# Performance work log

Hardware: AMD Instinct MI355X
Metric: run time of the kernel (lower is better)

## Reference

```python
import jax, jax.numpy as jnp
import numpy as np

T, H, I, E, K = 4096, 2048, 1408, 8, 2  # tokens, hidden, intermediate, experts, top_k


def setup_inputs() -> dict:
    key = jax.random.key(0)
    ks = jax.random.split(key, 6)
    hidden_states = jax.random.normal(ks[0], (T, H), dtype=jnp.float32)
    gate_weight = jax.random.normal(ks[1], (E, H), dtype=jnp.float32) * 0.02  # fp32 gate, per source assert
    w13_weight = jax.random.randint(ks[2], (E, 2 * I, H), -127, 128, dtype=jnp.int8)
    w13_weight_scale = jax.random.uniform(ks[3], (E, 2 * I), dtype=jnp.float32, minval=0.5, maxval=1.5) * 0.005
    w2_weight = jax.random.randint(ks[4], (E, H, I), -127, 128, dtype=jnp.int8)
    w2_weight_scale = jax.random.uniform(ks[5], (E, H), dtype=jnp.float32, minval=0.5, maxval=1.5) * 0.005
    return dict(hidden_states=hidden_states, gate_weight=gate_weight,
                w13_weight=w13_weight, w13_weight_scale=w13_weight_scale,
                w2_weight=w2_weight, w2_weight_scale=w2_weight_scale)


def _dynamic_quant_i8(x):
    # per-token dynamic symmetric int8: scale = max|x|/127 (smooth scales default to ones)
    s = jnp.maximum(jnp.max(jnp.abs(x), axis=-1, keepdims=True) / 127.0, 1e-8)
    q = jnp.clip(jnp.round(x / s), -127.0, 127.0)
    return q, s


def reference(hidden_states, gate_weight, w13_weight, w13_weight_scale, w2_weight, w2_weight_scale):
    # --- gating: fp32 linear + topk softmax (renormalize=True) ---
    logits = hidden_states @ gate_weight.T              # [T, E]
    probs = jax.nn.softmax(logits, axis=-1)
    topv, topi = jax.lax.top_k(probs, K)                # [T, K]
    gates = topv / jnp.sum(topv, axis=-1, keepdims=True)
    # dense routing weights [T, E]: gate value where expert selected, else 0
    route = jnp.zeros((T, E), hidden_states.dtype).at[jnp.arange(T)[:, None], topi].add(gates)

    # --- dynamic per-token int8 quant of routed input (same token value for each of its K copies) ---
    q_in, s_in = _dynamic_quant_i8(hidden_states)       # [T, H], [T, 1]

    # --- grouped w8a8 GEMM (fc1) -> SwiGLU -> requant -> grouped GEMM (fc2) -> weighted combine ---
    def step(acc, xs):
        w13, s13, w2, s2w, r = xs                       # per-expert weights / route column [T]
        h1 = (q_in @ w13.T.astype(jnp.float32)) * s_in * s13[None, :]   # dequant fc1: [T, 2I]
        g, u = h1[:, :I], h1[:, I:]
        act = jax.nn.silu(g) * u                        # SwiGLU
        q_a, s_a = _dynamic_quant_i8(act)
        h2 = (q_a @ w2.T.astype(jnp.float32)) * s_a * s2w[None, :]      # dequant fc2: [T, H]
        return acc + r[:, None] * h2, None

    acc0 = jnp.zeros_like(hidden_states)
    out, _ = jax.lax.scan(step, acc0,
                          (w13_weight, w13_weight_scale, w2_weight, w2_weight_scale, route.T))
    return out
```

## Files before the change

### kernel.cpp

```cpp
#include <hip/hip_runtime.h>

#define T_TOK 4096
#define H_DIM 2048
#define I_DIM 1408
#define E_NUM 8
#define NI2   (2 * I_DIM)

typedef int v4i __attribute__((ext_vector_type(4)));

#define GLD_LDS16(gptr, lptr)                                                        \
  __builtin_amdgcn_global_load_lds(                                                  \
      (const __attribute__((address_space(1))) void*)(gptr),                         \
      (__attribute__((address_space(3))) void*)(lptr), 16, 0, 0)

__global__ __launch_bounds__(256) void pack_all(const int* __restrict__ w13,
                                                const int* __restrict__ w2,
                                                signed char* __restrict__ qw13,
                                                signed char* __restrict__ qw2,
                                                int n16a, int n16tot) {
  int i = blockIdx.x * 256 + threadIdx.x;
  if (i >= n16tot) return;
  const int* src;
  signed char* dst;
  int j;
  if (i < n16a) { src = w13; dst = qw13; j = i; }
  else          { src = w2;  dst = qw2;  j = i - n16a; }
  const int4* s4 = (const int4*)src + (size_t)j * 4;
  int4 v0 = s4[0], v1 = s4[1], v2 = s4[2], v3 = s4[3];
  union { signed char c[16]; int4 v; } pk;
  pk.c[0] = (signed char)v0.x;  pk.c[1] = (signed char)v0.y;
  pk.c[2] = (signed char)v0.z;  pk.c[3] = (signed char)v0.w;
  pk.c[4] = (signed char)v1.x;  pk.c[5] = (signed char)v1.y;
  pk.c[6] = (signed char)v1.z;  pk.c[7] = (signed char)v1.w;
  pk.c[8] = (signed char)v2.x;  pk.c[9] = (signed char)v2.y;
  pk.c[10] = (signed char)v2.z; pk.c[11] = (signed char)v2.w;
  pk.c[12] = (signed char)v3.x; pk.c[13] = (signed char)v3.y;
  pk.c[14] = (signed char)v3.z; pk.c[15] = (signed char)v3.w;
  ((int4*)dst)[j] = pk.v;
}

__global__ __launch_bounds__(256) void gate_route_quant(
    const float* __restrict__ hs, const float* __restrict__ gw,
    signed char* __restrict__ qin, float* __restrict__ s_in,
    int* __restrict__ tope, float* __restrict__ gts) {
  const int t = blockIdx.x;
  const int tid = threadIdx.x;
  const int lane = tid & 63;
  const int wave = tid >> 6;
  const float* row = hs + (size_t)t * H_DIM;

  const float4* r4 = (const float4*)row + tid * 2;
  float4 xa = r4[0], xb = r4[1];
  float x[8] = {xa.x, xa.y, xa.z, xa.w, xb.x, xb.y, xb.z, xb.w};

  double pd[8];
  for (int e = 0; e < 8; e++) pd[e] = 0.0;
  float am = 0.f;
  for (int j = 0; j < 8; j++) {
    float v = x[j];
    am = fmaxf(am, fabsf(v));
    int col = tid * 8 + j;
    for (int e = 0; e < 8; e++)
      pd[e] += (double)v * (double)gw[e * H_DIM + col];
  }
  for (int e = 0; e < 8; e++)
    for (int s = 32; s; s >>= 1) pd[e] += __shfl_down(pd[e], s);
  for (int s = 32; s; s >>= 1) am = fmaxf(am, __shfl_down(am, s));

  __shared__ double sred[4][8];
  __shared__ float sam[4];
  __shared__ float sbc;
  if (lane == 0) {
    for (int e = 0; e < 8; e++) sred[wave][e] = pd[e];
    sam[wave] = am;
  }
  __syncthreads();
  if (tid == 0) {
    float l[8];
    for (int e = 0; e < 8; e++)
      l[e] = (float)(sred[0][e] + sred[1][e] + sred[2][e] + sred[3][e]);
    float amx = fmaxf(fmaxf(sam[0], sam[1]), fmaxf(sam[2], sam[3]));
    float s = fmaxf(amx / 127.0f, 1e-8f);
    s_in[t] = s;
    sbc = s;
    int i1 = 0;
    for (int e = 1; e < 8; e++) if (l[e] > l[i1]) i1 = e;
    int i2 = -1;
    for (int e = 0; e < 8; e++) {
      if (e == i1) continue;
      if (i2 < 0 || l[e] > l[i2]) i2 = e;
    }
    float d = expf(l[i2] - l[i1]);
    tope[2 * t] = i1;     gts[2 * t] = 1.0f / (1.0f + d);
    tope[2 * t + 1] = i2; gts[2 * t + 1] = d / (1.0f + d);
  }
  __syncthreads();
  float s = sbc;
  union { signed char c[8]; unsigned long long u; } pk;
  for (int j = 0; j < 8; j++) {
    float q = rintf(x[j] / s);
    q = fminf(127.f, fmaxf(-127.f, q));
    pk.c[j] = (signed char)q;
  }
  ((unsigned long long*)(qin + (size_t)t * H_DIM))[tid] = pk.u;
}

__global__ __launch_bounds__(256) void build_lists(
    const int* __restrict__ tope, int* __restrict__ tok_list,
    int* __restrict__ epos, int* __restrict__ cnt) {
  __shared__ int lc[E_NUM];
  __shared__ int lbase[E_NUM];
  const int tid = threadIdx.x;
  if (tid < E_NUM) lc[tid] = 0;
  __syncthreads();
  const int t = blockIdx.x * 256 + tid;
  int e0 = tope[2 * t], e1 = tope[2 * t + 1];
  int p0 = atomicAdd(&lc[e0], 1);
  int p1 = atomicAdd(&lc[e1], 1);
  __syncthreads();
  if (tid < E_NUM) lbase[tid] = atomicAdd(&cnt[tid], lc[tid]);
  __syncthreads();
  int pos0 = lbase[e0] + p0;
  int pos1 = lbase[e1] + p1;
  tok_list[e0 * T_TOK + pos0] = t;
  tok_list[e1 * T_TOK + pos1] = t;
  epos[2 * t] = (e0 << 16) | pos0;
  epos[2 * t + 1] = (e1 << 16) | pos1;
}

__global__ void calc_off(const int* __restrict__ cnt, int* __restrict__ off) {
  if (threadIdx.x == 0) {
    int s = 0;
    for (int e = 0; e < E_NUM; e++) { off[e] = s; s += cnt[e]; }
  }
}

__global__ __launch_bounds__(256, 4) void gemm1_silu(
    const signed char* __restrict__ qw13, const signed char* __restrict__ qin,
    const float* __restrict__ s_in, const float* __restrict__ s13,
    const int* __restrict__ tok_list, const int* __restrict__ cnt,
    const int* __restrict__ off, float* __restrict__ act,
    unsigned int* __restrict__ amax) {
  const int bid = blockIdx.x;
  const int e = bid & 7;
  const int xt = bid >> 9;
  const int yt = (bid >> 3) & 63;
  const int ce = cnt[e];
  const int m0 = yt * 64;
  if (m0 >= ce) return;
  const int n0 = xt * 64;

  __shared__ __align__(16) signed char As[64 * 64];
  __shared__ __align__(16) signed char Bg[64 * 64];
  __shared__ __align__(16) signed char Bu[64 * 64];

  const int tid = threadIdx.x;
  const int lane = tid & 63;
  const int wave = tid >> 6;
  const int quad = lane >> 4;
  const int ln = lane & 15;

  const int* tl = tok_list + e * T_TOK;
  const int rowA = tid >> 2;
  const int kc = (tid & 3) * 16;

  const int tA = tl[min(m0 + rowA, ce - 1)];
  const signed char* gA = qin + (size_t)tA * H_DIM + kc;
  const signed char* w13e = qw13 + (size_t)e * NI2 * H_DIM;
  const signed char* gBg = w13e + (size_t)(n0 + rowA) * H_DIM + kc;
  const signed char* gBu = gBg + (size_t)I_DIM * H_DIM;
  const int ldsA = tid * 16;

  v4i accg[4], accu[4];
  v4i zero = {0, 0, 0, 0};
#pragma unroll
  for (int i = 0; i < 4; i++) { accg[i] = zero; accu[i] = zero; }

  for (int k0 = 0; k0 < H_DIM; k0 += 64) {
    __syncthreads();
    GLD_LDS16(gA + k0, As + ldsA);
    GLD_LDS16(gBg + k0, Bg + ldsA);
    GLD_LDS16(gBu + k0, Bu + ldsA);
    __syncthreads();

    v4i af[4], bg, bu;
#pragma unroll
    for (int mt = 0; mt < 4; mt++)
      af[mt] = *(const v4i*)(As + (mt * 16 + ln) * 64 + quad * 16);
    bg = *(const v4i*)(Bg + (wave * 16 + ln) * 64 + quad * 16);
    bu = *(const v4i*)(Bu + (wave * 16 + ln) * 64 + quad * 16);
#pragma unroll
    for (int mt = 0; mt < 4; mt++) {
      accg[mt] = __builtin_amdgcn_mfma_i32_16x16x64_i8(af[mt], bg, accg[mt], 0, 0, 0);
      accu[mt] = __builtin_amdgcn_mfma_i32_16x16x64_i8(af[mt], bu, accu[mt], 0, 0, 0);
    }
  }

  const float* s13e = s13 + e * NI2;
  const int n = n0 + wave * 16 + ln;
  const float sgv = s13e[n];
  const float suv = s13e[I_DIM + n];
  const int offe = off[e];
#pragma unroll
  for (int mt = 0; mt < 4; mt++) {
#pragma unroll
    for (int r = 0; r < 4; r++) {
      int mrel = m0 + mt * 16 + quad * 4 + r;
      bool valid = mrel < ce;
      int tok = tl[valid ? mrel : 0];
      float si = s_in[tok];
      int crow = offe + mrel;
      float g = (float)accg[mt][r] * si * sgv;
      float u = (float)accu[mt][r] * si * suv;
      float a = g / (1.0f + expf(-g)) * u;
      if (valid) act[(size_t)crow * I_DIM + n] = a;
      float am = fabsf(a);
      for (int s = 1; s < 16; s <<= 1) am = fmaxf(am, __shfl_xor(am, s, 16));
      if (valid && ln == 0) atomicMax(amax + crow, __float_as_uint(am));
    }
  }
}

__global__ __launch_bounds__(256) void quant_act(const float* __restrict__ act,
                                                 const unsigned int* __restrict__ amax,
                                                 signed char* __restrict__ qa,
                                                 float* __restrict__ s_a) {
  const int r = blockIdx.x;
  float am = __uint_as_float(amax[r]);
  float s = fmaxf(am / 127.0f, 1e-8f);
  if (threadIdx.x == 0) s_a[r] = s;
  const float* arow = act + (size_t)r * I_DIM;
  signed char* qrow = qa + (size_t)r * I_DIM;
  for (int j = threadIdx.x; j < I_DIM; j += 256) {
    float q = rintf(arow[j] / s);
    q = fminf(127.f, fmaxf(-127.f, q));
    qrow[j] = (signed char)q;
  }
}

__global__ __launch_bounds__(256, 4) void gemm2_h2(
    const signed char* __restrict__ qw2, const signed char* __restrict__ qa,
    const float* __restrict__ s_a, const float* __restrict__ s2w,
    const int* __restrict__ cnt, const int* __restrict__ off,
    float* __restrict__ h2s) {
  const int bid = blockIdx.x;
  const int e = bid & 7;
  const int xt = bid >> 9;
  const int yt = (bid >> 3) & 63;
  const int ce = cnt[e];
  const int m0 = yt * 64;
  if (m0 >= ce) return;
  const int n0 = xt * 128;
  const int offe = off[e];

  __shared__ __align__(16) signed char As[64 * 64];
  __shared__ __align__(16) signed char Bs[128 * 64];

  const int tid = threadIdx.x;
  const int lane = tid & 63;
  const int wave = tid >> 6;
  const int quad = lane >> 4;
  const int ln = lane & 15;

  const int rowA = tid >> 2;
  const int kc = (tid & 3) * 16;

  const signed char* gA = qa + (size_t)(offe + min(m0 + rowA, ce - 1)) * I_DIM + kc;
  const signed char* w2e = qw2 + (size_t)e * H_DIM * I_DIM;
  const signed char* gB0 = w2e + (size_t)(n0 + rowA) * I_DIM + kc;
  const signed char* gB1 = gB0 + (size_t)64 * I_DIM;
  const int ldsA = tid * 16;
  const int lds1 = 4096 + ldsA;

  v4i acc[4][2];
  v4i zero = {0, 0, 0, 0};
#pragma unroll
  for (int i = 0; i < 4; i++)
#pragma unroll
    for (int j = 0; j < 2; j++) acc[i][j] = zero;

  for (int k0 = 0; k0 < I_DIM; k0 += 64) {
    __syncthreads();
    GLD_LDS16(gA + k0, As + ldsA);
    GLD_LDS16(gB0 + k0, Bs + ldsA);
    GLD_LDS16(gB1 + k0, Bs + lds1);
    __syncthreads();

    v4i af[4], bf[2];
#pragma unroll
    for (int mt = 0; mt < 4; mt++)
      af[mt] = *(const v4i*)(As + (mt * 16 + ln) * 64 + quad * 16);
#pragma unroll
    for (int nt = 0; nt < 2; nt++)
      bf[nt] = *(const v4i*)(Bs + (wave * 32 + nt * 16 + ln) * 64 + quad * 16);
#pragma unroll
    for (int mt = 0; mt < 4; mt++)
#pragma unroll
      for (int nt = 0; nt < 2; nt++)
        acc[mt][nt] = __builtin_amdgcn_mfma_i32_16x16x64_i8(af[mt], bf[nt], acc[mt][nt], 0, 0, 0);
  }

  const float* s2e = s2w + e * H_DIM;
  float sw[2];
  int ncol[2];
#pragma unroll
  for (int nt = 0; nt < 2; nt++) {
    int n = n0 + wave * 32 + nt * 16 + ln;
    ncol[nt] = n;
    sw[nt] = s2e[n];
  }
#pragma unroll
  for (int mt = 0; mt < 4; mt++) {
#pragma unroll
    for (int r = 0; r < 4; r++) {
      int mrel = m0 + mt * 16 + quad * 4 + r;
      if (mrel >= ce) continue;
      float sa = s_a[offe + mrel];
      float* orow = h2s + (size_t)(offe + mrel) * H_DIM;
#pragma unroll
      for (int nt = 0; nt < 2; nt++)
        orow[ncol[nt]] = (float)acc[mt][nt][r] * sa * sw[nt];
    }
  }
}

__global__ __launch_bounds__(256) void gather_out(
    const float* __restrict__ h2s, const int* __restrict__ epos,
    const float* __restrict__ gts, const int* __restrict__ off,
    float* __restrict__ out) {
  const int t = blockIdx.x;
  int a = epos[2 * t], b = epos[2 * t + 1];
  float g1 = gts[2 * t], g2 = gts[2 * t + 1];
  int r1 = off[a >> 16] + (a & 0xffff);
  int r2 = off[b >> 16] + (b & 0xffff);
  const float4* R1 = (const float4*)(h2s + (size_t)r1 * H_DIM);
  const float4* R2 = (const float4*)(h2s + (size_t)r2 * H_DIM);
  float4* O = (float4*)(out + (size_t)t * H_DIM);
  for (int c = threadIdx.x; c < H_DIM / 4; c += 256) {
    float4 x = R1[c], y = R2[c];
    float4 z;
    z.x = g1 * x.x + g2 * y.x;
    z.y = g1 * x.y + g2 * y.y;
    z.z = g1 * x.z + g2 * y.z;
    z.w = g1 * x.w + g2 * y.w;
    O[c] = z;
  }
}

extern "C" void kernel_launch(void* const* d_in, const int* in_sizes, int n_in,
                              void* d_out, int out_size, void* d_ws, size_t ws_size,
                              hipStream_t stream) {
  const float* hs = (const float*)d_in[0];
  const float* gw = (const float*)d_in[1];
  const int* w13 = (const int*)d_in[2];
  const float* s13 = (const float*)d_in[3];
  const int* w2 = (const int*)d_in[4];
  const float* s2w = (const float*)d_in[5];
  float* out = (float*)d_out;

  char* ws = (char*)d_ws;
  size_t o = 0;
  auto take = [&](size_t b) {
    char* p = ws + o;
    o += (b + 255) & ~(size_t)255;
    return p;
  };
  signed char* qw13 = (signed char*)take((size_t)E_NUM * NI2 * H_DIM);
  signed char* qin = (signed char*)take((size_t)T_TOK * H_DIM);
  float* act = (float*)take((size_t)T_TOK * 2 * I_DIM * 4);
  float* h2s = (float*)qw13;
  signed char* qw2 = (signed char*)take((size_t)E_NUM * H_DIM * I_DIM);
  signed char* qa = (signed char*)take((size_t)T_TOK * 2 * I_DIM);
  float* sin_ = (float*)take((size_t)T_TOK * 4);
  float* sa = (float*)take((size_t)T_TOK * 2 * 4);
  unsigned int* amax = (unsigned int*)take((size_t)T_TOK * 2 * 4);
  int* tokl = (int*)take((size_t)E_NUM * T_TOK * 4);
  int* tope = (int*)take((size_t)T_TOK * 2 * 4);
  int* epos = (int*)take((size_t)T_TOK * 2 * 4);
  float* gts = (float*)take((size_t)T_TOK * 2 * 4);
  int* cnt = (int*)take(E_NUM * 4);
  int* off = (int*)take(E_NUM * 4);

  hipMemsetAsync(amax, 0, (size_t)T_TOK * 2 * 4, stream);
  hipMemsetAsync(cnt, 0, (size_t)E_NUM * 4, stream);

  {
    int n16a = E_NUM * NI2 * H_DIM / 16;
    int n16b = E_NUM * H_DIM * I_DIM / 16;
    int n16tot = n16a + n16b;
    pack_all<<<(n16tot + 255) / 256, 256, 0, stream>>>(w13, w2, qw13, qw2, n16a, n16tot);
  }
  gate_route_quant<<<T_TOK, 256, 0, stream>>>(hs, gw, qin, sin_, tope, gts);
  build_lists<<<T_TOK / 256, 256, 0, stream>>>(tope, tokl, epos, cnt);
  calc_off<<<1, 64, 0, stream>>>(cnt, off);
  gemm1_silu<<<(I_DIM / 64) * 64 * E_NUM, 256, 0, stream>>>(qw13, qin, sin_, s13, tokl, cnt, off, act, amax);
  quant_act<<<T_TOK * 2, 256, 0, stream>>>(act, amax, qa, sa);
  gemm2_h2<<<(H_DIM / 128) * 64 * E_NUM, 256, 0, stream>>>(qw2, qa, sa, s2w, cnt, off, h2s);
  gather_out<<<T_TOK, 256, 0, stream>>>(h2s, epos, gts, off, out);
}
```

Baseline: 586.1 us.

## Double-buffer LDS tiles in both grouped GEMM kernels to overlap loads with MFMA

Both int8 GEMM kernels now keep two LDS buffers per operand and issue the global-to-LDS loads for the next K-step before running the MFMAs on the current one. This replaces the two barriers per iteration with one, so memory latency is meant to hide behind compute. It doubles LDS use per block, which may reduce occupancy, and relies on the single trailing barrier together with the LDS-DMA wait behaviour to order the async writes.

```diff
diff --git a/kernel.cpp b/kernel.cpp
--- a/kernel.cpp
+++ b/kernel.cpp
@@ -150,9 +150,9 @@
   if (m0 >= ce) return;
   const int n0 = xt * 64;
 
-  __shared__ __align__(16) signed char As[64 * 64];
-  __shared__ __align__(16) signed char Bg[64 * 64];
-  __shared__ __align__(16) signed char Bu[64 * 64];
+  __shared__ __align__(16) signed char As[2][64 * 64];
+  __shared__ __align__(16) signed char Bg[2][64 * 64];
+  __shared__ __align__(16) signed char Bu[2][64 * 64];
 
   const int tid = threadIdx.x;
   const int lane = tid & 63;
@@ -176,24 +176,33 @@
 #pragma unroll
   for (int i = 0; i < 4; i++) { accg[i] = zero; accu[i] = zero; }
 
-  for (int k0 = 0; k0 < H_DIM; k0 += 64) {
-    __syncthreads();
-    GLD_LDS16(gA + k0, As + ldsA);
-    GLD_LDS16(gBg + k0, Bg + ldsA);
-    GLD_LDS16(gBu + k0, Bu + ldsA);
-    __syncthreads();
-
+  GLD_LDS16(gA, &As[0][ldsA]);
+  GLD_LDS16(gBg, &Bg[0][ldsA]);
+  GLD_LDS16(gBu, &Bu[0][ldsA]);
+  __syncthreads();
+
+  const int NK = H_DIM / 64;
+  int cur = 0;
+  for (int kk = 0; kk < NK; ++kk) {
+    if (kk + 1 < NK) {
+      const int k0 = (kk + 1) * 64;
+      GLD_LDS16(gA + k0, &As[cur ^ 1][ldsA]);
+      GLD_LDS16(gBg + k0, &Bg[cur ^ 1][ldsA]);
+      GLD_LDS16(gBu + k0, &Bu[cur ^ 1][ldsA]);
+    }
     v4i af[4], bg, bu;
 #pragma unroll
     for (int mt = 0; mt < 4; mt++)
-      af[mt] = *(const v4i*)(As + (mt * 16 + ln) * 64 + quad * 16);
-    bg = *(const v4i*)(Bg + (wave * 16 + ln) * 64 + quad * 16);
-    bu = *(const v4i*)(Bu + (wave * 16 + ln) * 64 + quad * 16);
+      af[mt] = *(const v4i*)(&As[cur][(mt * 16 + ln) * 64 + quad * 16]);
+    bg = *(const v4i*)(&Bg[cur][(wave * 16 + ln) * 64 + quad * 16]);
+    bu = *(const v4i*)(&Bu[cur][(wave * 16 + ln) * 64 + quad * 16]);
 #pragma unroll
     for (int mt = 0; mt < 4; mt++) {
       accg[mt] = __builtin_amdgcn_mfma_i32_16x16x64_i8(af[mt], bg, accg[mt], 0, 0, 0);
       accu[mt] = __builtin_amdgcn_mfma_i32_16x16x64_i8(af[mt], bu, accu[mt], 0, 0, 0);
     }
+    __syncthreads();
+    cur ^= 1;
   }
 
   const float* s13e = s13 + e * NI2;
@@ -253,8 +262,8 @@
   const int n0 = xt * 128;
   const int offe = off[e];
 
-  __shared__ __align__(16) signed char As[64 * 64];
-  __shared__ __align__(16) signed char Bs[128 * 64];
+  __shared__ __align__(16) signed char As[2][64 * 64];
+  __shared__ __align__(16) signed char Bs[2][128 * 64];
 
   const int tid = threadIdx.x;
   const int lane = tid & 63;
@@ -270,7 +279,6 @@
   const signed char* gB0 = w2e + (size_t)(n0 + rowA) * I_DIM + kc;
   const signed char* gB1 = gB0 + (size_t)64 * I_DIM;
   const int ldsA = tid * 16;
-  const int lds1 = 4096 + ldsA;
 
   v4i acc[4][2];
   v4i zero = {0, 0, 0, 0};
@@ -279,25 +287,34 @@
 #pragma unroll
     for (int j = 0; j < 2; j++) acc[i][j] = zero;
 
-  for (int k0 = 0; k0 < I_DIM; k0 += 64) {
-    __syncthreads();
-    GLD_LDS16(gA + k0, As + ldsA);
-    GLD_LDS16(gB0 + k0, Bs + ldsA);
-    GLD_LDS16(gB1 + k0, Bs + lds1);
-    __syncthreads();
-
+  GLD_LDS16(gA, &As[0][ldsA]);
+  GLD_LDS16(gB0, &Bs[0][ldsA]);
+  GLD_LDS16(gB1, &Bs[0][4096 + ldsA]);
+  __syncthreads();
+
+  const int NK = I_DIM / 64;
+  int cur = 0;
+  for (int kk = 0; kk < NK; ++kk) {
+    if (kk + 1 < NK) {
+      const int k0 = (kk + 1) * 64;
+      GLD_LDS16(gA + k0, &As[cur ^ 1][ldsA]);
+      GLD_LDS16(gB0 + k0, &Bs[cur ^ 1][ldsA]);
+      GLD_LDS16(gB1 + k0, &Bs[cur ^ 1][4096 + ldsA]);
+    }
     v4i af[4], bf[2];
 #pragma unroll
     for (int mt = 0; mt < 4; mt++)
-      af[mt] = *(const v4i*)(As + (mt * 16 + ln) * 64 + quad * 16);
+      af[mt] = *(const v4i*)(&As[cur][(mt * 16 + ln) * 64 + quad * 16]);
 #pragma unroll
     for (int nt = 0; nt < 2; nt++)
-      bf[nt] = *(const v4i*)(Bs + (wave * 32 + nt * 16 + ln) * 64 + quad * 16);
+      bf[nt] = *(const v4i*)(&Bs[cur][(wave * 32 + nt * 16 + ln) * 64 + quad * 16]);
 #pragma unroll
     for (int mt = 0; mt < 4; mt++)
 #pragma unroll
       for (int nt = 0; nt < 2; nt++)
         acc[mt][nt] = __builtin_amdgcn_mfma_i32_16x16x64_i8(af[mt], bf[nt], acc[mt][nt], 0, 0, 0);
+    __syncthreads();
+    cur ^= 1;
   }
 
   const float* s2e = s2w + e * H_DIM;
```

Measured after the change: 598.7 us. 1.02x slower.

## Triple-buffer LDS with async global-to-LDS prefetch in both grouped GEMMs

Applied to the files above, without the earlier changes.

Replaces the single-buffered, twice-synchronised K loop in both int8 GEMM kernels with a three-stage ring of LDS buffers. Global-to-LDS loads for the tile two steps ahead are issued before computing the current tile, and vmcnt waits plus a single barrier per iteration replace the two __syncthreads. The goal is to hide global load latency behind MFMA work. In exchange, LDS use per block triples (36KB in gemm1, 36KB in gemm2), which may reduce occupancy below the launch-bounds target of 4 blocks per CU, and correctness depends on the hand-written vmcnt counts.

```diff
diff --git a/kernel.cpp b/kernel.cpp
--- a/kernel.cpp
+++ b/kernel.cpp
@@ -12,6 +12,9 @@
   __builtin_amdgcn_global_load_lds(                                                  \
       (const __attribute__((address_space(1))) void*)(gptr),                         \
       (__attribute__((address_space(3))) void*)(lptr), 16, 0, 0)
+
+#define RECYCLE_BARRIER() asm volatile("s_waitcnt lgkmcnt(0)\n\ts_barrier" ::: "memory")
+#define SCHED_FENCE() __builtin_amdgcn_sched_barrier(0)
 
 __global__ __launch_bounds__(256) void pack_all(const int* __restrict__ w13,
                                                 const int* __restrict__ w2,
@@ -150,9 +153,9 @@
   if (m0 >= ce) return;
   const int n0 = xt * 64;
 
-  __shared__ __align__(16) signed char As[64 * 64];
-  __shared__ __align__(16) signed char Bg[64 * 64];
-  __shared__ __align__(16) signed char Bu[64 * 64];
+  __shared__ __align__(16) signed char As[3][64 * 64];
+  __shared__ __align__(16) signed char Bg[3][64 * 64];
+  __shared__ __align__(16) signed char Bu[3][64 * 64];
 
   const int tid = threadIdx.x;
   const int lane = tid & 63;
@@ -176,25 +179,51 @@
 #pragma unroll
   for (int i = 0; i < 4; i++) { accg[i] = zero; accu[i] = zero; }
 
-  for (int k0 = 0; k0 < H_DIM; k0 += 64) {
-    __syncthreads();
-    GLD_LDS16(gA + k0, As + ldsA);
-    GLD_LDS16(gBg + k0, Bg + ldsA);
-    GLD_LDS16(gBu + k0, Bu + ldsA);
-    __syncthreads();
-
+  auto STAGE = [&](int b, int k0) {
+    GLD_LDS16(gA + k0, &As[b][ldsA]);
+    GLD_LDS16(gBg + k0, &Bg[b][ldsA]);
+    GLD_LDS16(gBu + k0, &Bu[b][ldsA]);
+  };
+  auto COMPUTE = [&](int c) {
     v4i af[4], bg, bu;
 #pragma unroll
     for (int mt = 0; mt < 4; mt++)
-      af[mt] = *(const v4i*)(As + (mt * 16 + ln) * 64 + quad * 16);
-    bg = *(const v4i*)(Bg + (wave * 16 + ln) * 64 + quad * 16);
-    bu = *(const v4i*)(Bu + (wave * 16 + ln) * 64 + quad * 16);
+      af[mt] = *(const v4i*)(&As[c][(mt * 16 + ln) * 64 + quad * 16]);
+    bg = *(const v4i*)(&Bg[c][(wave * 16 + ln) * 64 + quad * 16]);
+    bu = *(const v4i*)(&Bu[c][(wave * 16 + ln) * 64 + quad * 16]);
 #pragma unroll
     for (int mt = 0; mt < 4; mt++) {
       accg[mt] = __builtin_amdgcn_mfma_i32_16x16x64_i8(af[mt], bg, accg[mt], 0, 0, 0);
       accu[mt] = __builtin_amdgcn_mfma_i32_16x16x64_i8(af[mt], bu, accu[mt], 0, 0, 0);
     }
-  }
+  };
+
+  const int NK = H_DIM / 64;
+  STAGE(0, 0);
+  STAGE(1, 64);
+  int cur = 0, stg = 2;
+  for (int kk = 0; kk < NK - 2; ++kk) {
+    SCHED_FENCE();
+    RECYCLE_BARRIER();
+    STAGE(stg, (kk + 2) * 64);
+    asm volatile("s_waitcnt vmcnt(6)" ::: "memory");
+    asm volatile("s_barrier" ::: "memory");
+    SCHED_FENCE();
+    COMPUTE(cur);
+    cur = (cur == 2) ? 0 : cur + 1;
+    stg = (stg == 2) ? 0 : stg + 1;
+  }
+  SCHED_FENCE();
+  asm volatile("s_waitcnt vmcnt(3)" ::: "memory");
+  asm volatile("s_barrier" ::: "memory");
+  SCHED_FENCE();
+  COMPUTE(cur);
+  cur = (cur == 2) ? 0 : cur + 1;
+  SCHED_FENCE();
+  asm volatile("s_waitcnt vmcnt(0)" ::: "memory");
+  asm volatile("s_barrier" ::: "memory");
+  SCHED_FENCE();
+  COMPUTE(cur);
 
   const float* s13e = s13 + e * NI2;
   const int n = n0 + wave * 16 + ln;
@@ -253,8 +282,8 @@
   const int n0 = xt * 128;
   const int offe = off[e];
 
-  __shared__ __align__(16) signed char As[64 * 64];
-  __shared__ __align__(16) signed char Bs[128 * 64];
+  __shared__ __align__(16) signed char As[3][64 * 64];
+  __shared__ __align__(16) signed char Bs[3][128 * 64];
 
   const int tid = threadIdx.x;
   const int lane = tid & 63;
@@ -270,7 +299,6 @@
   const signed char* gB0 = w2e + (size_t)(n0 + rowA) * I_DIM + kc;
   const signed char* gB1 = gB0 + (size_t)64 * I_DIM;
   const int ldsA = tid * 16;
-  const int lds1 = 4096 + ldsA;
 
   v4i acc[4][2];
   v4i zero = {0, 0, 0, 0};
@@ -279,26 +307,52 @@
 #pragma unroll
     for (int j = 0; j < 2; j++) acc[i][j] = zero;
 
-  for (int k0 = 0; k0 < I_DIM; k0 += 64) {
-    __syncthreads();
-    GLD_LDS16(gA + k0, As + ldsA);
-    GLD_LDS16(gB0 + k0, Bs + ldsA);
-    GLD_LDS16(gB1 + k0, Bs + lds1);
-    __syncthreads();
-
+  auto STAGE = [&](int b, int k0) {
+    GLD_LDS16(gA + k0, &As[b][ldsA]);
+    GLD_LDS16(gB0 + k0, &Bs[b][ldsA]);
+    GLD_LDS16(gB1 + k0, &Bs[b][4096 + ldsA]);
+  };
+  auto COMPUTE = [&](int c) {
     v4i af[4], bf[2];
 #pragma unroll
     for (int mt = 0; mt < 4; mt++)
-      af[mt] = *(const v4i*)(As + (mt * 16 + ln) * 64 + quad * 16);
+      af[mt] = *(const v4i*)(&As[c][(mt * 16 + ln) * 64 + quad * 16]);
 #pragma unroll
     for (int nt = 0; nt < 2; nt++)
-      bf[nt] = *(const v4i*)(Bs + (wave * 32 + nt * 16 + ln) * 64 + quad * 16);
+      bf[nt] = *(const v4i*)(&Bs[c][(wave * 32 + nt * 16 + ln) * 64 + quad * 16]);
 #pragma unroll
     for (int mt = 0; mt < 4; mt++)
 #pragma unroll
       for (int nt = 0; nt < 2; nt++)
         acc[mt][nt] = __builtin_amdgcn_mfma_i32_16x16x64_i8(af[mt], bf[nt], acc[mt][nt], 0, 0, 0);
-  }
+  };
+
+  const int NK = I_DIM / 64;
+  STAGE(0, 0);
+  STAGE(1, 64);
+  int cur = 0, stg = 2;
+  for (int kk = 0; kk < NK - 2; ++kk) {
+    SCHED_FENCE();
+    RECYCLE_BARRIER();
+    STAGE(stg, (kk + 2) * 64);
+    asm volatile("s_waitcnt vmcnt(6)" ::: "memory");
+    asm volatile("s_barrier" ::: "memory");
+    SCHED_FENCE();
+    COMPUTE(cur);
+    cur = (cur == 2) ? 0 : cur + 1;
+    stg = (stg == 2) ? 0 : stg + 1;
+  }
+  SCHED_FENCE();
+  asm volatile("s_waitcnt vmcnt(3)" ::: "memory");
+  asm volatile("s_barrier" ::: "memory");
+  SCHED_FENCE();
+  COMPUTE(cur);
+  cur = (cur == 2) ? 0 : cur + 1;
+  SCHED_FENCE();
+  asm volatile("s_waitcnt vmcnt(0)" ::: "memory");
+  asm volatile("s_barrier" ::: "memory");
+  SCHED_FENCE();
+  COMPUTE(cur);
 
   const float* s2e = s2w + e * H_DIM;
   float sw[2];
```

Result: slower. 605.2 us (+3.3%).
